# Performance work log

Measured on AMD Instinct MI355X. Metric: run time of the kernel, lower is better.

The kernel has to match this reference:

```python
import jax, jax.numpy as jnp
import numpy as np

NUM_HEADS = 8
DIM_HEAD = 64
GROUPS = 32
EPS = 1e-5


def setup_inputs() -> dict:
    key = jax.random.key(0)
    k1, k2, k3 = jax.random.split(key, 3)
    C = 512
    inner = NUM_HEADS * DIM_HEAD  # 512
    x = jax.random.normal(k1, (8, C, 32, 32), dtype=jnp.float32)
    gamma = jnp.ones((C,), dtype=jnp.float32)
    beta = jnp.zeros((C,), dtype=jnp.float32)
    w_qkv = jax.random.normal(k2, (3 * inner, C), dtype=jnp.float32) * 0.02
    w_out = jax.random.normal(k3, (C, inner), dtype=jnp.float32) * 0.02
    return {"x": x, "gamma": gamma, "beta": beta, "w_qkv": w_qkv, "w_out": w_out}


def group_norm(x, gamma, beta):
    b, c, h, w = x.shape
    xg = x.reshape(b, GROUPS, c // GROUPS, h, w)
    mean = jnp.mean(xg, axis=(2, 3, 4), keepdims=True)
    var = jnp.var(xg, axis=(2, 3, 4), keepdims=True)
    xn = ((xg - mean) * jax.lax.rsqrt(var + EPS)).reshape(b, c, h, w)
    return xn * gamma[None, :, None, None] + beta[None, :, None, None]


def reference(x, gamma, beta, w_qkv, w_out):
    b, c, h, w = x.shape
    H, d = NUM_HEADS, DIM_HEAD
    inner = H * d
    scale = d ** (-0.5)
    residual = x
    xn = group_norm(x, gamma, beta)
    # 1x1 conv (no bias) == channel matmul
    qkv = jnp.einsum('bchw,oc->bohw', xn, w_qkv)  # [b, 3*inner, h, w]
    q, k, v = jnp.split(qkv, 3, axis=1)
    def to_heads(t):
        # b (H d) h w -> b H (h w) d
        return t.reshape(b, H, d, h * w).transpose(0, 1, 3, 2)
    q, k, v = to_heads(q), to_heads(k), to_heads(v)
    attn = jnp.einsum('bhid,bhjd->bhij', q, k) * scale  # [b,H,hw,hw]
    attn = jax.nn.softmax(attn, axis=-1)
    out = jnp.einsum('bhij,bhjd->bhid', attn, v)  # [b,H,hw,d]
    # b H (h w) d -> b (H d) h w
    out = out.transpose(0, 1, 3, 2).reshape(b, inner, h, w)
    out = jnp.einsum('bchw,oc->bohw', out, w_out)
    return out + residual
```

## Files before the change

kernel.cpp:

```cpp
#include <hip/hip_runtime.h>


typedef __attribute__((ext_vector_type(8))) short bf16x8;
typedef __attribute__((ext_vector_type(4))) short bf16x4;
typedef __attribute__((ext_vector_type(4))) float f32x4;

#define NB 8
#define NC 512
#define HW 1024
#define NHEAD 8
#define DHEAD 64
#define GROUPS 32
#define CPG 16
#define QKV_N 1536

#define GLL16(gaddr, ldsaddr)                                                  \
    __builtin_amdgcn_global_load_lds(                                          \
        (const __attribute__((address_space(1))) unsigned*)(gaddr),            \
        (__attribute__((address_space(3))) unsigned*)(ldsaddr), 16, 0, 0)

__device__ alignas(64) short g_xn[(size_t)8192 * 512];
__device__ alignas(64) short g_qkv[(size_t)8192 * 1536];
__device__ alignas(64) short g_vt[(size_t)64 * 64 * 1024];
__device__ alignas(64) short g_attno[(size_t)8192 * 512];
__device__ alignas(64) short g_wqkv[(size_t)1536 * 512];
__device__ alignas(64) short g_wout[(size_t)512 * 512];

__device__ __forceinline__ float b2f(short h) {
    union { unsigned u; float f; } v;
    v.u = ((unsigned)(unsigned short)h) << 16;
    return v.f;
}
__device__ __forceinline__ short f2b(float f) {
    union { float f; unsigned u; } v;
    v.f = f;
    unsigned r = v.u + 0x7fff + ((v.u >> 16) & 1);
    return (short)(r >> 16);
}

__global__ __launch_bounds__(256) void prep_kernel(
    const float* __restrict__ x, const float* __restrict__ gamma,
    const float* __restrict__ beta, const float* __restrict__ wqkv,
    const float* __restrict__ wout) {
    int tid = threadIdx.x;
    if (blockIdx.x >= 256) {
        int wb = blockIdx.x - 256;
        for (int i = wb * 256 + tid; i < 1536 * 512; i += 64 * 256) {
            float v = wqkv[i];
            if (i < 512 * 512) v *= 0.125f;
            g_wqkv[i] = f2b(v);
        }
        for (int i = wb * 256 + tid; i < 512 * 512; i += 64 * 256)
            g_wout[i] = f2b(wout[i]);
        return;
    }
    int b = blockIdx.x >> 5, g = blockIdx.x & 31;
    __shared__ alignas(16) short tile[CPG][HW];
    __shared__ float red[2][4];
    __shared__ float sg[CPG], sb[CPG];
    if (tid < CPG) {
        int cg = g * CPG + tid;
        sg[tid] = gamma[cg];
        sb[tid] = beta[cg];
    }
    const float* xb = x + (size_t)b * NC * HW + (size_t)g * CPG * HW;
    float s1 = 0.f, s2 = 0.f;
    #pragma unroll
    for (int it = 0; it < 8; it++) {
        int idx = tid + it * 256;
        f32x4 v0 = *(const f32x4*)(xb + idx * 8);
        f32x4 v1 = *(const f32x4*)(xb + idx * 8 + 4);
        bf16x8 w;
        #pragma unroll
        for (int j = 0; j < 4; j++) {
            s1 += v0[j] + v1[j]; s2 += v0[j] * v0[j] + v1[j] * v1[j];
            w[j] = f2b(v0[j]); w[j + 4] = f2b(v1[j]);
        }
        *(bf16x8*)(&((short*)tile)[idx * 8]) = w;
    }
    #pragma unroll
    for (int off = 32; off; off >>= 1) { s1 += __shfl_xor(s1, off); s2 += __shfl_xor(s2, off); }
    int wid = tid >> 6;
    if ((tid & 63) == 0) { red[0][wid] = s1; red[1][wid] = s2; }
    __syncthreads();
    float t1 = red[0][0] + red[0][1] + red[0][2] + red[0][3];
    float t2 = red[1][0] + red[1][1] + red[1][2] + red[1][3];
    float mean = t1 * (1.f / 16384.f);
    float var  = t2 * (1.f / 16384.f) - mean * mean;
    float inv  = rsqrtf(var + 1e-5f);
    #pragma unroll
    for (int p = 0; p < 4; p++) {
        int s = tid * 4 + p;
        bf16x8 pk0, pk1;
        #pragma unroll
        for (int cc = 0; cc < 8; cc++) {
            pk0[cc] = f2b((b2f(tile[cc][s])     - mean) * inv * sg[cc]     + sb[cc]);
            pk1[cc] = f2b((b2f(tile[cc + 8][s]) - mean) * inv * sg[cc + 8] + sb[cc + 8]);
        }
        size_t dst = ((size_t)(b * HW + s)) * NC + g * CPG;
        *(bf16x8*)(g_xn + dst)     = pk0;
        *(bf16x8*)(g_xn + dst + 8) = pk1;
    }
}

__global__ __launch_bounds__(256) void gemm_qkv() {
    const int K = NC;
    int tid = threadIdx.x, lane = tid & 63, wid = tid >> 6;
    int quad = lane >> 4, l15 = lane & 15;
    int row0 = blockIdx.x * 128;
    int col0 = blockIdx.y * 128;
    __shared__ alignas(16) short sa[128 * 32];
    __shared__ alignas(16) short sbuf[128 * 32];
    int srow = wid * 32 + (lane >> 2);
    int scol = (lane & 3) * 8;
    const short* ga = g_xn   + (size_t)(row0 + srow) * K + scol;
    const short* gb = g_wqkv + (size_t)(col0 + srow) * K + scol;
    short* la = sa   + wid * 1024;
    short* lb = sbuf + wid * 1024;
    int mw = (wid >> 1) * 64, nw = (wid & 1) * 64;
    f32x4 acc[4][4] = {};
    for (int k = 0; k < K; k += 32) {
        GLL16(ga + k, la);
        GLL16(ga + (size_t)16 * K + k, la + 512);
        GLL16(gb + k, lb);
        GLL16(gb + (size_t)16 * K + k, lb + 512);
        __syncthreads();
        bf16x8 af[4], bfv[4];
        #pragma unroll
        for (int m = 0; m < 4; m++) af[m]  = *(const bf16x8*)&sa[(mw + m * 16 + l15) * 32 + quad * 8];
        #pragma unroll
        for (int n = 0; n < 4; n++) bfv[n] = *(const bf16x8*)&sbuf[(nw + n * 16 + l15) * 32 + quad * 8];
        #pragma unroll
        for (int m = 0; m < 4; m++)
            #pragma unroll
            for (int n = 0; n < 4; n++)
                acc[m][n] = __builtin_amdgcn_mfma_f32_16x16x32_bf16(af[m], bfv[n], acc[m][n], 0, 0, 0);
        __syncthreads();
    }
    #pragma unroll
    for (int m = 0; m < 4; m++)
        #pragma unroll
        for (int n = 0; n < 4; n++)
            #pragma unroll
            for (int r = 0; r < 4; r++) {
                int row = row0 + mw + m * 16 + quad * 4 + r;
                int col = col0 + nw + n * 16 + l15;
                g_qkv[(size_t)row * QKV_N + col] = f2b(acc[m][n][r]);
            }
}

__global__ __launch_bounds__(256) void transpose_v() {
    int bh = blockIdx.x & 63, st = blockIdx.x >> 6;
    int b = bh >> 3, h = bh & 7;
    int tid = threadIdx.x;
    __shared__ alignas(16) short tile[64][72];
    int s0 = st * 64;
    #pragma unroll
    for (int cc = 0; cc < 2; cc++) {
        int idx = tid + cc * 256;
        int s = idx >> 3, dc = idx & 7;
        *(bf16x8*)&tile[s][dc * 8] =
            *(const bf16x8*)(g_qkv + ((size_t)(b * HW + s0 + s)) * QKV_N + 1024 + h * DHEAD + dc * 8);
    }
    __syncthreads();
    #pragma unroll
    for (int cc = 0; cc < 2; cc++) {
        int idx = tid + cc * 256;
        int d = idx & 63, sc = idx >> 6;
        bf16x8 o;
        #pragma unroll
        for (int j = 0; j < 8; j++) o[j] = tile[sc * 8 + j][d];
        *(bf16x8*)(g_vt + ((size_t)(bh * 64 + d)) * HW + s0 + sc * 8) = o;
    }
}

__global__ __launch_bounds__(256) void attn_kernel() {
    int bh = blockIdx.x & 63, qt = blockIdx.x >> 6;
    int b = bh >> 3, h = bh & 7;
    int tid = threadIdx.x, lane = tid & 63, wid = tid >> 6;
    int quad = lane >> 4, l15 = lane & 15;
    __shared__ alignas(16) short kt[2][64 * 64];
    __shared__ alignas(16) short vt[2][64 * 64];
    __shared__ alignas(16) short pt4[4][16][16][4];
    int qrow0 = qt * 64 + wid * 16;

    const short* qb = g_qkv + ((size_t)(b * HW + qrow0 + l15)) * QKV_N + h * DHEAD + quad * 8;
    bf16x8 aq0 = *(const bf16x8*)qb;
    bf16x8 aq1 = *(const bf16x8*)(qb + 32);
    f32x4 acc_o[4] = {};
    float l_part = 0.f;

    int r_lo = lane >> 3;
    int s_log = (lane & 7) ^ r_lo;
    int swz = l15 & 7;

    auto stage = [&](int it, int bufi) {
        int t0 = it * 64;
        #pragma unroll
        for (int c = 0; c < 2; c++) {
            int r = wid * 16 + c * 8 + r_lo;
            GLL16(g_qkv + ((size_t)(b * HW + t0 + r)) * QKV_N + 512 + h * DHEAD + s_log * 8,
                  &kt[bufi][(wid * 16 + c * 8) * 64]);
            GLL16(g_vt + ((size_t)(bh * 64 + r)) * HW + t0 + s_log * 8,
                  &vt[bufi][(wid * 16 + c * 8) * 64]);
        }
    };

    stage(0, 0);
    __syncthreads();
    for (int it = 0; it < 16; it++) {
        int cur = it & 1;
        if (it < 15) stage(it + 1, cur ^ 1);
        #pragma unroll
        for (int sub = 0; sub < 4; sub++) {
            int row = sub * 16 + l15;
            bf16x8 k0 = *(const bf16x8*)&kt[cur][row * 64 + ((quad ^ swz) * 8)];
            bf16x8 k1 = *(const bf16x8*)&kt[cur][row * 64 + (((4 + quad) ^ swz) * 8)];
            f32x4 z = {};
            z = __builtin_amdgcn_mfma_f32_16x16x32_bf16(k0, aq0, z, 0, 0, 0);
            z = __builtin_amdgcn_mfma_f32_16x16x32_bf16(k1, aq1, z, 0, 0, 0);
            unsigned u[4];
            #pragma unroll
            for (int r = 0; r < 4; r++) {
                float e = __expf(z[r]);
                l_part += e;
                union { float f; unsigned b; } cv; cv.f = e;
                u[r] = cv.b + 0x8000u;
            }
            union { unsigned w[2]; bf16x4 s; } pk;
            pk.w[0] = (u[0] >> 16) | (u[1] & 0xffff0000u);
            pk.w[1] = (u[2] >> 16) | (u[3] & 0xffff0000u);
            *(bf16x4*)&pt4[wid][sub * 4 + quad][l15][0] = pk.s;
        }
        asm volatile("" ::: "memory");
        bf16x8 ap0, ap1;
        {
            union { bf16x4 hh[2]; bf16x8 v; } cc;
            cc.hh[0] = *(const bf16x4*)&pt4[wid][quad * 2][l15][0];
            cc.hh[1] = *(const bf16x4*)&pt4[wid][quad * 2 + 1][l15][0];
            ap0 = cc.v;
            cc.hh[0] = *(const bf16x4*)&pt4[wid][8 + quad * 2][l15][0];
            cc.hh[1] = *(const bf16x4*)&pt4[wid][8 + quad * 2 + 1][l15][0];
            ap1 = cc.v;
        }
        #pragma unroll
        for (int nd = 0; nd < 4; nd++) {
            int row = nd * 16 + l15;
            bf16x8 bv0 = *(const bf16x8*)&vt[cur][row * 64 + ((quad ^ swz) * 8)];
            bf16x8 bv1 = *(const bf16x8*)&vt[cur][row * 64 + (((4 + quad) ^ swz) * 8)];
            acc_o[nd] = __builtin_amdgcn_mfma_f32_16x16x32_bf16(ap0, bv0, acc_o[nd], 0, 0, 0);
            acc_o[nd] = __builtin_amdgcn_mfma_f32_16x16x32_bf16(ap1, bv1, acc_o[nd], 0, 0, 0);
        }
        __syncthreads();
    }
    float lf = l_part;
    lf += __shfl_xor(lf, 16); lf += __shfl_xor(lf, 32);
    #pragma unroll
    for (int r = 0; r < 4; r++) {
        float lr = __shfl(lf, quad * 4 + r);
        float invl = 1.f / lr;
        size_t row = (size_t)(b * HW + qrow0 + quad * 4 + r);
        #pragma unroll
        for (int nd = 0; nd < 4; nd++)
            g_attno[row * NC + h * DHEAD + nd * 16 + l15] = f2b(acc_o[nd][r] * invl);
    }
}

__global__ __launch_bounds__(256) void gemm_out(
    const float* __restrict__ xres, float* __restrict__ out) {
    const int K = NC;
    int tid = threadIdx.x, lane = tid & 63, wid = tid >> 6;
    int quad = lane >> 4, l15 = lane & 15;
    int row0 = blockIdx.x * 128;
    int col0 = blockIdx.y * 128;
    __shared__ alignas(16) short sa[128 * 32];
    __shared__ alignas(16) short sbuf[128 * 32];
    int srow = wid * 32 + (lane >> 2);
    int scol = (lane & 3) * 8;
    const short* ga = g_wout  + (size_t)(row0 + srow) * K + scol;
    const short* gb = g_attno + (size_t)(col0 + srow) * K + scol;
    short* la = sa   + wid * 1024;
    short* lb = sbuf + wid * 1024;
    int mw = (wid >> 1) * 64, nw = (wid & 1) * 64;
    f32x4 acc[4][4] = {};
    for (int k = 0; k < K; k += 32) {
        GLL16(ga + k, la);
        GLL16(ga + (size_t)16 * K + k, la + 512);
        GLL16(gb + k, lb);
        GLL16(gb + (size_t)16 * K + k, lb + 512);
        __syncthreads();
        bf16x8 af[4], bfv[4];
        #pragma unroll
        for (int m = 0; m < 4; m++) af[m]  = *(const bf16x8*)&sa[(mw + m * 16 + l15) * 32 + quad * 8];
        #pragma unroll
        for (int n = 0; n < 4; n++) bfv[n] = *(const bf16x8*)&sbuf[(nw + n * 16 + l15) * 32 + quad * 8];
        #pragma unroll
        for (int m = 0; m < 4; m++)
            #pragma unroll
            for (int n = 0; n < 4; n++)
                acc[m][n] = __builtin_amdgcn_mfma_f32_16x16x32_bf16(af[m], bfv[n], acc[m][n], 0, 0, 0);
        __syncthreads();
    }
    #pragma unroll
    for (int m = 0; m < 4; m++)
        #pragma unroll
        for (int n = 0; n < 4; n++)
            #pragma unroll
            for (int r = 0; r < 4; r++) {
                int o  = row0 + mw + m * 16 + quad * 4 + r;
                int bs = col0 + nw + n * 16 + l15;
                size_t addr = (size_t)(bs >> 10) * ((size_t)NC * HW) + (size_t)o * HW + (bs & 1023);
                out[addr] = acc[m][n][r] + xres[addr];
            }
}

extern "C" void kernel_launch(void* const* d_in, const int* in_sizes, int n_in,
                              void* d_out, int out_size, void* d_ws, size_t ws_size,
                              hipStream_t stream) {
    const float* x     = (const float*)d_in[0];
    const float* gamma = (const float*)d_in[1];
    const float* beta  = (const float*)d_in[2];
    const float* wqkv  = (const float*)d_in[3];
    const float* wout  = (const float*)d_in[4];
    float* out = (float*)d_out;

    prep_kernel<<<dim3(320), dim3(256), 0, stream>>>(x, gamma, beta, wqkv, wout);
    gemm_qkv<<<dim3(64, 12), dim3(256), 0, stream>>>();
    transpose_v<<<dim3(1024), dim3(256), 0, stream>>>();
    attn_kernel<<<dim3(1024), dim3(256), 0, stream>>>();
    gemm_out<<<dim3(4, 64), dim3(256), 0, stream>>>(x, out);
}
```

Measured before the change: 160.4 us.

## Rewrite QKV GEMM with 256x256 tiles and 4-stage LDS prefetch pipeline

Result: slower. 166.9 us (+4.1%).

```diff
diff --git a/kernel.cpp b/kernel.cpp
--- a/kernel.cpp
+++ b/kernel.cpp
@@ -103,49 +103,103 @@
     }
 }
 
-__global__ __launch_bounds__(256) void gemm_qkv() {
+__global__ __launch_bounds__(512, 2) void gemm_qkv() {
     const int K = NC;
-    int tid = threadIdx.x, lane = tid & 63, wid = tid >> 6;
+    int tid = threadIdx.x, lane = tid & 63, w = tid >> 6;
     int quad = lane >> 4, l15 = lane & 15;
-    int row0 = blockIdx.x * 128;
-    int col0 = blockIdx.y * 128;
-    __shared__ alignas(16) short sa[128 * 32];
-    __shared__ alignas(16) short sbuf[128 * 32];
-    int srow = wid * 32 + (lane >> 2);
-    int scol = (lane & 3) * 8;
-    const short* ga = g_xn   + (size_t)(row0 + srow) * K + scol;
-    const short* gb = g_wqkv + (size_t)(col0 + srow) * K + scol;
-    short* la = sa   + wid * 1024;
-    short* lb = sbuf + wid * 1024;
-    int mw = (wid >> 1) * 64, nw = (wid & 1) * 64;
-    f32x4 acc[4][4] = {};
-    for (int k = 0; k < K; k += 32) {
-        GLL16(ga + k, la);
-        GLL16(ga + (size_t)16 * K + k, la + 512);
-        GLL16(gb + k, lb);
-        GLL16(gb + (size_t)16 * K + k, lb + 512);
-        __syncthreads();
-        bf16x8 af[4], bfv[4];
-        #pragma unroll
-        for (int m = 0; m < 4; m++) af[m]  = *(const bf16x8*)&sa[(mw + m * 16 + l15) * 32 + quad * 8];
-        #pragma unroll
-        for (int n = 0; n < 4; n++) bfv[n] = *(const bf16x8*)&sbuf[(nw + n * 16 + l15) * 32 + quad * 8];
-        #pragma unroll
-        for (int m = 0; m < 4; m++)
-            #pragma unroll
-            for (int n = 0; n < 4; n++)
-                acc[m][n] = __builtin_amdgcn_mfma_f32_16x16x32_bf16(af[m], bfv[n], acc[m][n], 0, 0, 0);
-        __syncthreads();
-    }
-    #pragma unroll
-    for (int m = 0; m < 4; m++)
-        #pragma unroll
-        for (int n = 0; n < 4; n++)
+    int wm = w >> 2, wn = w & 3;
+    int m0   = blockIdx.x * 256;
+    int col0 = blockIdx.y * 256;
+    __shared__ alignas(16) short lds[4][2][256 * 32];
+
+    int rA = lane >> 2;
+    int gr = (lane & 3) * 8;
+    const short* gA = g_xn   + (size_t)m0   * K;
+    const short* gB = g_wqkv + (size_t)col0 * K;
+
+    auto stageA = [&](int slot, int kt) {
+        int k0 = kt * 32;
+        #pragma unroll
+        for (int j = 0; j < 2; j++) {
+            int r = j * 128 + w * 16 + rA;
+            GLL16(gA + (size_t)r * K + k0 + gr,
+                  &lds[slot][0][(j * 128 + w * 16) * 32]);
+        }
+    };
+    auto stageB = [&](int slot, int kt) {
+        int k0 = kt * 32;
+        #pragma unroll
+        for (int j = 0; j < 2; j++) {
+            int r = j * 128 + w * 16 + rA;
+            GLL16(gB + (size_t)r * K + k0 + gr,
+                  &lds[slot][1][(j * 128 + w * 16) * 32]);
+        }
+    };
+
+    stageA(0, 0); stageB(0, 0);
+    stageA(1, 1); stageB(1, 1);
+    stageA(2, 2); stageB(2, 2);
+    asm volatile("s_waitcnt vmcnt(8)" ::: "memory");
+    __builtin_amdgcn_s_barrier();
+    asm volatile("" ::: "memory");
+
+    f32x4 acc[8][4] = {};
+    for (int t = 0; t < 16; t++) {
+        int st    = t & 3;
+        int pf    = t + 3;
+        int pslot = pf & 3;
+        int psrc  = (pf < 16) ? pf : 15;
+        bf16x8 af[4], bfr[4], af2[4];
+
+        #pragma unroll
+        for (int fr = 0; fr < 4; fr++)
+            af[fr]  = *(const bf16x8*)&lds[st][0][(wm * 128 + fr * 16 + l15) * 32 + quad * 8];
+        #pragma unroll
+        for (int fc = 0; fc < 4; fc++)
+            bfr[fc] = *(const bf16x8*)&lds[st][1][(wn * 64  + fc * 16 + l15) * 32 + quad * 8];
+        stageA(pslot, psrc);
+        asm volatile("" ::: "memory");
+        __builtin_amdgcn_s_barrier();
+        asm volatile("" ::: "memory");
+        __builtin_amdgcn_s_setprio(1);
+        #pragma unroll
+        for (int fr = 0; fr < 4; fr++)
+            #pragma unroll
+            for (int fc = 0; fc < 4; fc++)
+                acc[fr][fc] = __builtin_amdgcn_mfma_f32_16x16x32_bf16(af[fr], bfr[fc], acc[fr][fc], 0, 0, 0);
+        __builtin_amdgcn_s_setprio(0);
+        asm volatile("" ::: "memory");
+        __builtin_amdgcn_s_barrier();
+        asm volatile("" ::: "memory");
+
+        #pragma unroll
+        for (int fr = 0; fr < 4; fr++)
+            af2[fr] = *(const bf16x8*)&lds[st][0][(wm * 128 + 64 + fr * 16 + l15) * 32 + quad * 8];
+        stageB(pslot, psrc);
+        asm volatile("s_waitcnt vmcnt(8)" ::: "memory");
+        __builtin_amdgcn_s_barrier();
+        asm volatile("" ::: "memory");
+        __builtin_amdgcn_s_setprio(1);
+        #pragma unroll
+        for (int fr = 0; fr < 4; fr++)
+            #pragma unroll
+            for (int fc = 0; fc < 4; fc++)
+                acc[4 + fr][fc] = __builtin_amdgcn_mfma_f32_16x16x32_bf16(af2[fr], bfr[fc], acc[4 + fr][fc], 0, 0, 0);
+        __builtin_amdgcn_s_setprio(0);
+        asm volatile("" ::: "memory");
+        __builtin_amdgcn_s_barrier();
+        asm volatile("" ::: "memory");
+    }
+
+    #pragma unroll
+    for (int fr = 0; fr < 8; fr++)
+        #pragma unroll
+        for (int fc = 0; fc < 4; fc++)
             #pragma unroll
             for (int r = 0; r < 4; r++) {
-                int row = row0 + mw + m * 16 + quad * 4 + r;
-                int col = col0 + nw + n * 16 + l15;
-                g_qkv[(size_t)row * QKV_N + col] = f2b(acc[m][n][r]);
+                int row = m0 + wm * 128 + fr * 16 + quad * 4 + r;
+                int col = col0 + wn * 64 + fc * 16 + l15;
+                g_qkv[(size_t)row * QKV_N + col] = f2b(acc[fr][fc][r]);
             }
 }
 
@@ -325,7 +379,7 @@
     float* out = (float*)d_out;
 
     prep_kernel<<<dim3(320), dim3(256), 0, stream>>>(x, gamma, beta, wqkv, wout);
-    gemm_qkv<<<dim3(64, 12), dim3(256), 0, stream>>>();
+    gemm_qkv<<<dim3(32, 6), dim3(512), 0, stream>>>();
     transpose_v<<<dim3(1024), dim3(256), 0, stream>>>();
     attn_kernel<<<dim3(1024), dim3(256), 0, stream>>>();
     gemm_out<<<dim3(4, 64), dim3(256), 0, stream>>>(x, out);
```
